# Kernel optimization log

Measured on AMD Instinct MI355X. Metric: run time of the kernel, lower is better.

The kernel has to match this reference:

```python
import jax, jax.numpy as jnp
import numpy as np

PAD = (2, 2)  # from kernel=[1,3,3,1], sampling_factor_padding=2, kernel_size=3


def _make_kernel(k1d):
    k = np.asarray(k1d, dtype=np.float32)
    k2d = k[None, :] * k[:, None]
    return jnp.asarray(k2d / k2d.sum())


def setup_inputs() -> dict:
    key = jax.random.key(0)
    x = jax.random.normal(key, (8, 256, 256, 256), dtype=jnp.float32)
    kernel = _make_kernel([1, 3, 3, 1])  # [4,4] normalized FIR kernel (buffer)
    return {"x": x, "kernel": kernel}


def reference(x, kernel):
    # upfirdn2d with up=1, down=1, pad=(2,2): pad then depthwise TRUE convolution
    # (StyleGAN2 flips the kernel before F.conv2d, i.e. real convolution).
    B, C, H, W = x.shape
    kh, kw = kernel.shape
    w = jnp.flip(kernel, (0, 1)).astype(x.dtype)[None, None]  # [1,1,kh,kw]
    w = jnp.broadcast_to(w, (C, 1, kh, kw))  # depthwise: same kernel per channel
    out = jax.lax.conv_general_dilated(
        x, w,
        window_strides=(1, 1),
        padding=(PAD, PAD),
        dimension_numbers=("NCHW", "OIHW", "NCHW"),
        feature_group_count=C,
    )  # [B, C, H+1, W+1] since H + 4 - 4 + 1 = H + 1
    return out
```

## Files before the change

### kernel.cpp

```cpp
#include <hip/hip_runtime.h>


#define IW 256
#define IH 256
#define OW 257
#define OH 257
#define HSTR 260
#define NSLOT 35

typedef float f4u __attribute__((vector_size(16), aligned(4)));

__device__ __forceinline__ float sbc(float v) {
    return __uint_as_float(__builtin_amdgcn_readfirstlane(__float_as_uint(v)));
}

__global__ __launch_bounds__(512) void blur_fir_kernel(
    const float* __restrict__ x,
    const float* __restrict__ k2d,
    float* __restrict__ out,
    int ntasks, int nstride)
{
    __shared__ float Hs[NSLOT * HSTR];

    const int lane = threadIdx.x & 63;
    const int wv   = threadIdx.x >> 6;

    const float w0 = sbc(k2d[0]);
    const float w1 = sbc(k2d[1]);
    const float w2 = sbc(k2d[2]);
    const float w3 = sbc(k2d[3]);
    const float inv = 1.0f / w0;
    const float v1 = sbc(k2d[4]  * inv);
    const float v2 = sbc(k2d[8]  * inv);
    const float v3 = sbc(k2d[12] * inv);

    const int   c0 = lane << 2;
    const float mL = (lane > 0)  ? 1.0f : 0.0f;
    const float mR = (lane < 63) ? 1.0f : 0.0f;
    const int   lm = (lane > 0)  ? lane - 1 : 0;
    const int   lp = (lane < 63) ? lane + 1 : 63;
    const bool last = (lane == 63);

    for (int t = blockIdx.x; t < ntasks; t += nstride) {
        const int plane = t >> 3;
        const int rg    = t & 7;
        const int a     = rg << 5;
        const float* xp = x + ((size_t)plane << 16);

        __syncthreads();

        #pragma unroll
        for (int j = wv; j < NSLOT; j += 8) {
            const int r = a - 2 + j;
            int rr = min(max(r, 0), IH - 1);
            float4 Bv = *(const float4*)(xp + (rr << 8) + c0);
            float rm = (r >= 0 && r < IH) ? 1.0f : 0.0f;
            float lx = __shfl(Bv.z, lm, 64) * mL;
            float ly = __shfl(Bv.w, lm, 64) * mL;
            float rv = __shfl(Bv.x, lp, 64) * mR;
            float4 h;
            h.x = w0 * Bv.y + w1 * Bv.x + w2 * ly   + w3 * lx;
            h.y = w0 * Bv.z + w1 * Bv.y + w2 * Bv.x + w3 * ly;
            h.z = w0 * Bv.w + w1 * Bv.z + w2 * Bv.y + w3 * Bv.x;
            h.w = w0 * rv   + w1 * Bv.w + w2 * Bv.z + w3 * Bv.y;
            float h4 = (w2 * Bv.w + w3 * Bv.z) * rm;
            h.x *= rm; h.y *= rm; h.z *= rm; h.w *= rm;
            float* hp = Hs + j * HSTR;
            *(float4*)(hp + c0) = h;
            if (last) hp[256] = h4;
        }
        __syncthreads();

        const int j0 = wv << 2;
        const float* hb = Hs + j0 * HSTR + c0;
        float4 h0 = *(const float4*)(hb           );
        float4 h1 = *(const float4*)(hb +     HSTR);
        float4 h2 = *(const float4*)(hb + 2 * HSTR);
        float4 h3 = *(const float4*)(hb + 3 * HSTR);
        float4 h4 = *(const float4*)(hb + 4 * HSTR);
        float4 h5 = *(const float4*)(hb + 5 * HSTR);
        float4 h6 = *(const float4*)(hb + 6 * HSTR);

        auto vcomb = [&](float4 A, float4 B, float4 C, float4 D) -> float4 {
            float4 r;
            r.x = A.x + v1 * B.x + v2 * C.x + v3 * D.x;
            r.y = A.y + v1 * B.y + v2 * C.y + v3 * D.y;
            r.z = A.z + v1 * B.z + v2 * C.z + v3 * D.z;
            r.w = A.w + v1 * B.w + v2 * C.w + v3 * D.w;
            return r;
        };

        float* op = out + (size_t)plane * (OW * OH)
                        + (size_t)(a + (wv << 2)) * OW + c0;
        float4 R0 = vcomb(h3, h2, h1, h0);
        float4 R1 = vcomb(h4, h3, h2, h1);
        float4 R2 = vcomb(h5, h4, h3, h2);
        float4 R3 = vcomb(h6, h5, h4, h3);
        *(f4u*)(op         ) = (f4u){R0.x, R0.y, R0.z, R0.w};
        *(f4u*)(op +     OW) = (f4u){R1.x, R1.y, R1.z, R1.w};
        *(f4u*)(op + 2 * OW) = (f4u){R2.x, R2.y, R2.z, R2.w};
        *(f4u*)(op + 3 * OW) = (f4u){R3.x, R3.y, R3.z, R3.w};
        if (last) {
            const float* sp = Hs + j0 * HSTR + 256;
            float s0 = sp[0],        s1 = sp[HSTR],     s2 = sp[2 * HSTR];
            float s3 = sp[3 * HSTR], s4 = sp[4 * HSTR], s5 = sp[5 * HSTR];
            float s6 = sp[6 * HSTR];
            op[4]          = s3 + v1 * s2 + v2 * s1 + v3 * s0;
            op[OW + 4]     = s4 + v1 * s3 + v2 * s2 + v3 * s1;
            op[2 * OW + 4] = s5 + v1 * s4 + v2 * s3 + v3 * s2;
            op[3 * OW + 4] = s6 + v1 * s5 + v2 * s4 + v3 * s3;
        }

        if (rg == 7 && wv == 7) {
            float4 Hm2 = *(const float4*)(Hs + 32 * HSTR + c0);
            float4 Hm1 = *(const float4*)(Hs + 33 * HSTR + c0);
            float4 R;
            R.x = v2 * Hm1.x + v3 * Hm2.x;
            R.y = v2 * Hm1.y + v3 * Hm2.y;
            R.z = v2 * Hm1.z + v3 * Hm2.z;
            R.w = v2 * Hm1.w + v3 * Hm2.w;
            *(f4u*)(op + 4 * OW) = (f4u){R.x, R.y, R.z, R.w};
            if (last)
                op[4 * OW + 4] = v2 * Hs[33 * HSTR + 256] + v3 * Hs[32 * HSTR + 256];
        }
    }
}

extern "C" void kernel_launch(void* const* d_in, const int* in_sizes, int n_in,
                              void* d_out, int out_size, void* d_ws, size_t ws_size,
                              hipStream_t stream) {
    const float* x   = (const float*)d_in[0];
    const float* k2d = (const float*)d_in[1];
    float* out = (float*)d_out;

    int nplanes = in_sizes[0] >> 16;
    int ntasks  = nplanes * 8;
    int nblocks = 1024;

    blur_fir_kernel<<<nblocks, 512, 0, stream>>>(x, k2d, out, ntasks, nblocks);
}
```

Measured before the change: 210.4 us.

## Prefetch next task's input rows into registers across loop iterations

Software-pipelines the persistent loop. The global loads for the next task are issued right after the shared-memory fill barrier, so they overlap the vertical pass and the output stores of the current task. The horizontal filter is computed in registers before the first barrier. This hides global load latency at the cost of higher register pressure (five float4 prefetch registers plus five horizontal results), which could reduce occupancy at 512 threads.

```diff
diff --git a/kernel.cpp b/kernel.cpp
--- a/kernel.cpp
+++ b/kernel.cpp
@@ -41,35 +41,72 @@
     const int   lp = (lane < 63) ? lane + 1 : 63;
     const bool last = (lane == 63);
 
-    for (int t = blockIdx.x; t < ntasks; t += nstride) {
+    const int  j4ok = (wv + 32 < NSLOT);
+
+    auto issue = [&](int tt, float4& G0, float4& G1, float4& G2,
+                     float4& G3, float4& G4) {
+        const int plane = tt >> 3;
+        const int a     = (tt & 7) << 5;
+        const float* xp = x + ((size_t)plane << 16);
+        auto ld = [&](int j) -> float4 {
+            int r  = a - 2 + j;
+            int rr = min(max(r, 0), IH - 1);
+            return *(const float4*)(xp + (rr << 8) + c0);
+        };
+        G0 = ld(wv);
+        G1 = ld(wv + 8);
+        G2 = ld(wv + 16);
+        G3 = ld(wv + 24);
+        G4 = j4ok ? ld(wv + 32) : G3;
+    };
+
+    int t = blockIdx.x;
+    float4 G0, G1, G2, G3, G4;
+    if (t < ntasks) issue(t, G0, G1, G2, G3, G4);
+
+    for (; t < ntasks; t += nstride) {
         const int plane = t >> 3;
         const int rg    = t & 7;
         const int a     = rg << 5;
-        const float* xp = x + ((size_t)plane << 16);
+
+        float4 Hv[5]; float h4s[5];
+        {
+            auto hc = [&](float4 Bv, int r, float4& h, float& h4) {
+                float rm = (r >= 0 && r < IH) ? 1.0f : 0.0f;
+                float lx = __shfl(Bv.z, lm, 64) * mL;
+                float ly = __shfl(Bv.w, lm, 64) * mL;
+                float rv = __shfl(Bv.x, lp, 64) * mR;
+                h.x = w0 * Bv.y + w1 * Bv.x + w2 * ly   + w3 * lx;
+                h.y = w0 * Bv.z + w1 * Bv.y + w2 * Bv.x + w3 * ly;
+                h.z = w0 * Bv.w + w1 * Bv.z + w2 * Bv.y + w3 * Bv.x;
+                h.w = w0 * rv   + w1 * Bv.w + w2 * Bv.z + w3 * Bv.y;
+                h4  = (w2 * Bv.w + w3 * Bv.z) * rm;
+                h.x *= rm; h.y *= rm; h.z *= rm; h.w *= rm;
+            };
+            hc(G0, a - 2 + wv,      Hv[0], h4s[0]);
+            hc(G1, a - 2 + wv + 8,  Hv[1], h4s[1]);
+            hc(G2, a - 2 + wv + 16, Hv[2], h4s[2]);
+            hc(G3, a - 2 + wv + 24, Hv[3], h4s[3]);
+            hc(G4, a - 2 + wv + 32, Hv[4], h4s[4]);
+        }
 
         __syncthreads();
 
         #pragma unroll
-        for (int j = wv; j < NSLOT; j += 8) {
-            const int r = a - 2 + j;
-            int rr = min(max(r, 0), IH - 1);
-            float4 Bv = *(const float4*)(xp + (rr << 8) + c0);
-            float rm = (r >= 0 && r < IH) ? 1.0f : 0.0f;
-            float lx = __shfl(Bv.z, lm, 64) * mL;
-            float ly = __shfl(Bv.w, lm, 64) * mL;
-            float rv = __shfl(Bv.x, lp, 64) * mR;
-            float4 h;
-            h.x = w0 * Bv.y + w1 * Bv.x + w2 * ly   + w3 * lx;
-            h.y = w0 * Bv.z + w1 * Bv.y + w2 * Bv.x + w3 * ly;
-            h.z = w0 * Bv.w + w1 * Bv.z + w2 * Bv.y + w3 * Bv.x;
-            h.w = w0 * rv   + w1 * Bv.w + w2 * Bv.z + w3 * Bv.y;
-            float h4 = (w2 * Bv.w + w3 * Bv.z) * rm;
-            h.x *= rm; h.y *= rm; h.z *= rm; h.w *= rm;
-            float* hp = Hs + j * HSTR;
-            *(float4*)(hp + c0) = h;
-            if (last) hp[256] = h4;
+        for (int k = 0; k < 5; ++k) {
+            const int j = wv + (k << 3);
+            if (k < 4 || j4ok) {
+                float* hp = Hs + j * HSTR;
+                *(float4*)(hp + c0) = Hv[k];
+                if (last) hp[256] = h4s[k];
+            }
         }
         __syncthreads();
+
+        {
+            int tn = t + nstride;
+            if (tn < ntasks) issue(tn, G0, G1, G2, G3, G4);
+        }
 
         const int j0 = wv << 2;
         const float* hb = Hs + j0 * HSTR + c0;
```

After: 214.9 us. 1.02x slower.

## Stream whole planes per block through a ring buffer of filtered rows

Applied to the files above, without the earlier changes.

Each block now walks an entire plane in eight sequential 32-row chunks instead of taking independent row-group tasks. Horizontally filtered rows live in a 36-slot shared-memory ring, so the three halo rows are reused from the previous chunk rather than reloaded and refiltered. Each chunk's global loads are issued before the barrier, which lets them overlap with other waves still finishing the previous chunk's output. The cost is more modular index arithmetic, uneven per-wave row counts in the first chunk, and fewer independent tasks for the scheduler to spread across the device.

```diff
diff --git a/kernel.cpp b/kernel.cpp
--- a/kernel.cpp
+++ b/kernel.cpp
@@ -6,7 +6,7 @@
 #define OW 257
 #define OH 257
 #define HSTR 260
-#define NSLOT 35
+#define RING 36
 
 typedef float f4u __attribute__((vector_size(16), aligned(4)));
 
@@ -18,9 +18,9 @@
     const float* __restrict__ x,
     const float* __restrict__ k2d,
     float* __restrict__ out,
-    int ntasks, int nstride)
+    int nplanes, int pstride)
 {
-    __shared__ float Hs[NSLOT * HSTR];
+    __shared__ float Hs[RING * HSTR];
 
     const int lane = threadIdx.x & 63;
     const int wv   = threadIdx.x >> 6;
@@ -41,87 +41,113 @@
     const int   lp = (lane < 63) ? lane + 1 : 63;
     const bool last = (lane == 63);
 
-    for (int t = blockIdx.x; t < ntasks; t += nstride) {
-        const int plane = t >> 3;
-        const int rg    = t & 7;
-        const int a     = rg << 5;
-        const float* xp = x + ((size_t)plane << 16);
+    for (int plane = blockIdx.x; plane < nplanes; plane += pstride) {
+        const float* xp   = x   + ((size_t)plane << 16);
+        float*       outp = out + (size_t)plane * (OW * OH);
 
-        __syncthreads();
+        for (int k = 0; k < 8; ++k) {
+            const int a = k << 5;
 
-        #pragma unroll
-        for (int j = wv; j < NSLOT; j += 8) {
-            const int r = a - 2 + j;
-            int rr = min(max(r, 0), IH - 1);
-            float4 Bv = *(const float4*)(xp + (rr << 8) + c0);
-            float rm = (r >= 0 && r < IH) ? 1.0f : 0.0f;
-            float lx = __shfl(Bv.z, lm, 64) * mL;
-            float ly = __shfl(Bv.w, lm, 64) * mL;
-            float rv = __shfl(Bv.x, lp, 64) * mR;
-            float4 h;
-            h.x = w0 * Bv.y + w1 * Bv.x + w2 * ly   + w3 * lx;
-            h.y = w0 * Bv.z + w1 * Bv.y + w2 * Bv.x + w3 * ly;
-            h.z = w0 * Bv.w + w1 * Bv.z + w2 * Bv.y + w3 * Bv.x;
-            h.w = w0 * rv   + w1 * Bv.w + w2 * Bv.z + w3 * Bv.y;
-            float h4 = (w2 * Bv.w + w3 * Bv.z) * rm;
-            h.x *= rm; h.y *= rm; h.z *= rm; h.w *= rm;
-            float* hp = Hs + j * HSTR;
-            *(float4*)(hp + c0) = h;
-            if (last) hp[256] = h4;
-        }
-        __syncthreads();
+            int n0, cnt;
+            if (k == 0) {
+                n0  = (wv < 3) ? (5 * wv - 2) : ((wv << 2) + 1);
+                cnt = (wv < 3) ? 5 : 4;
+            } else {
+                n0  = a + 1 + (wv << 2);
+                cnt = 4;
+            }
 
-        const int j0 = wv << 2;
-        const float* hb = Hs + j0 * HSTR + c0;
-        float4 h0 = *(const float4*)(hb           );
-        float4 h1 = *(const float4*)(hb +     HSTR);
-        float4 h2 = *(const float4*)(hb + 2 * HSTR);
-        float4 h3 = *(const float4*)(hb + 3 * HSTR);
-        float4 h4 = *(const float4*)(hb + 4 * HSTR);
-        float4 h5 = *(const float4*)(hb + 5 * HSTR);
-        float4 h6 = *(const float4*)(hb + 6 * HSTR);
+            float4 Bv[5];
+            #pragma unroll
+            for (int q = 0; q < 5; ++q) {
+                if (q < cnt) {
+                    int r  = n0 + q;
+                    int rr = min(max(r, 0), IH - 1);
+                    Bv[q] = *(const float4*)(xp + (rr << 8) + c0);
+                }
+            }
 
-        auto vcomb = [&](float4 A, float4 B, float4 C, float4 D) -> float4 {
-            float4 r;
-            r.x = A.x + v1 * B.x + v2 * C.x + v3 * D.x;
-            r.y = A.y + v1 * B.y + v2 * C.y + v3 * D.y;
-            r.z = A.z + v1 * B.z + v2 * C.z + v3 * D.z;
-            r.w = A.w + v1 * B.w + v2 * C.w + v3 * D.w;
-            return r;
-        };
+            __syncthreads();
 
-        float* op = out + (size_t)plane * (OW * OH)
-                        + (size_t)(a + (wv << 2)) * OW + c0;
-        float4 R0 = vcomb(h3, h2, h1, h0);
-        float4 R1 = vcomb(h4, h3, h2, h1);
-        float4 R2 = vcomb(h5, h4, h3, h2);
-        float4 R3 = vcomb(h6, h5, h4, h3);
-        *(f4u*)(op         ) = (f4u){R0.x, R0.y, R0.z, R0.w};
-        *(f4u*)(op +     OW) = (f4u){R1.x, R1.y, R1.z, R1.w};
-        *(f4u*)(op + 2 * OW) = (f4u){R2.x, R2.y, R2.z, R2.w};
-        *(f4u*)(op + 3 * OW) = (f4u){R3.x, R3.y, R3.z, R3.w};
-        if (last) {
-            const float* sp = Hs + j0 * HSTR + 256;
-            float s0 = sp[0],        s1 = sp[HSTR],     s2 = sp[2 * HSTR];
-            float s3 = sp[3 * HSTR], s4 = sp[4 * HSTR], s5 = sp[5 * HSTR];
-            float s6 = sp[6 * HSTR];
-            op[4]          = s3 + v1 * s2 + v2 * s1 + v3 * s0;
-            op[OW + 4]     = s4 + v1 * s3 + v2 * s2 + v3 * s1;
-            op[2 * OW + 4] = s5 + v1 * s4 + v2 * s3 + v3 * s2;
-            op[3 * OW + 4] = s6 + v1 * s5 + v2 * s4 + v3 * s3;
-        }
+            const int s0 = (n0 + 2) % RING;
+            #pragma unroll
+            for (int q = 0; q < 5; ++q) {
+                if (q < cnt) {
+                    const int r = n0 + q;
+                    float rm = (r >= 0 && r < IH) ? 1.0f : 0.0f;
+                    float4 B = Bv[q];
+                    float lx = __shfl(B.z, lm, 64) * mL;
+                    float ly = __shfl(B.w, lm, 64) * mL;
+                    float rv = __shfl(B.x, lp, 64) * mR;
+                    float4 h;
+                    h.x = w0 * B.y + w1 * B.x + w2 * ly  + w3 * lx;
+                    h.y = w0 * B.z + w1 * B.y + w2 * B.x + w3 * ly;
+                    h.z = w0 * B.w + w1 * B.z + w2 * B.y + w3 * B.x;
+                    h.w = w0 * rv  + w1 * B.w + w2 * B.z + w3 * B.y;
+                    float h4 = (w2 * B.w + w3 * B.z) * rm;
+                    h.x *= rm; h.y *= rm; h.z *= rm; h.w *= rm;
+                    int sq = s0 + q; if (sq >= RING) sq -= RING;
+                    float* hp = Hs + sq * HSTR;
+                    *(float4*)(hp + c0) = h;
+                    if (last) hp[256] = h4;
+                }
+            }
+            __syncthreads();
 
-        if (rg == 7 && wv == 7) {
-            float4 Hm2 = *(const float4*)(Hs + 32 * HSTR + c0);
-            float4 Hm1 = *(const float4*)(Hs + 33 * HSTR + c0);
-            float4 R;
-            R.x = v2 * Hm1.x + v3 * Hm2.x;
-            R.y = v2 * Hm1.y + v3 * Hm2.y;
-            R.z = v2 * Hm1.z + v3 * Hm2.z;
-            R.w = v2 * Hm1.w + v3 * Hm2.w;
-            *(f4u*)(op + 4 * OW) = (f4u){R.x, R.y, R.z, R.w};
-            if (last)
-                op[4 * OW + 4] = v2 * Hs[33 * HSTR + 256] + v3 * Hs[32 * HSTR + 256];
+            const int t0 = (a + (wv << 2)) % RING;
+            float4 h[7];
+            #pragma unroll
+            for (int q = 0; q < 7; ++q) {
+                int sq = t0 + q; if (sq >= RING) sq -= RING;
+                h[q] = *(const float4*)(Hs + sq * HSTR + c0);
+            }
+
+            auto vcomb = [&](float4 A, float4 B, float4 C, float4 D) -> float4 {
+                float4 r;
+                r.x = A.x + v1 * B.x + v2 * C.x + v3 * D.x;
+                r.y = A.y + v1 * B.y + v2 * C.y + v3 * D.y;
+                r.z = A.z + v1 * B.z + v2 * C.z + v3 * D.z;
+                r.w = A.w + v1 * B.w + v2 * C.w + v3 * D.w;
+                return r;
+            };
+
+            float* op = outp + (size_t)(a + (wv << 2)) * OW + c0;
+            float4 R0 = vcomb(h[3], h[2], h[1], h[0]);
+            float4 R1 = vcomb(h[4], h[3], h[2], h[1]);
+            float4 R2 = vcomb(h[5], h[4], h[3], h[2]);
+            float4 R3 = vcomb(h[6], h[5], h[4], h[3]);
+            *(f4u*)(op         ) = (f4u){R0.x, R0.y, R0.z, R0.w};
+            *(f4u*)(op +     OW) = (f4u){R1.x, R1.y, R1.z, R1.w};
+            *(f4u*)(op + 2 * OW) = (f4u){R2.x, R2.y, R2.z, R2.w};
+            *(f4u*)(op + 3 * OW) = (f4u){R3.x, R3.y, R3.z, R3.w};
+            if (last) {
+                float s[7];
+                #pragma unroll
+                for (int q = 0; q < 7; ++q) {
+                    int sq = t0 + q; if (sq >= RING) sq -= RING;
+                    s[q] = Hs[sq * HSTR + 256];
+                }
+                op[4]          = s[3] + v1 * s[2] + v2 * s[1] + v3 * s[0];
+                op[OW + 4]     = s[4] + v1 * s[3] + v2 * s[2] + v3 * s[1];
+                op[2 * OW + 4] = s[5] + v1 * s[4] + v2 * s[3] + v3 * s[2];
+                op[3 * OW + 4] = s[6] + v1 * s[5] + v2 * s[4] + v3 * s[3];
+            }
+
+            if (k == 7 && wv == 7) {
+                const int sA = 256 % RING;
+                const int sB = 257 % RING;
+                float4 Hm2 = *(const float4*)(Hs + sA * HSTR + c0);
+                float4 Hm1 = *(const float4*)(Hs + sB * HSTR + c0);
+                float4 R;
+                R.x = v2 * Hm1.x + v3 * Hm2.x;
+                R.y = v2 * Hm1.y + v3 * Hm2.y;
+                R.z = v2 * Hm1.z + v3 * Hm2.z;
+                R.w = v2 * Hm1.w + v3 * Hm2.w;
+                float* o2 = outp + (size_t)256 * OW + c0;
+                *(f4u*)o2 = (f4u){R.x, R.y, R.z, R.w};
+                if (last)
+                    o2[4] = v2 * Hs[sB * HSTR + 256] + v3 * Hs[sA * HSTR + 256];
+            }
         }
     }
 }
@@ -134,8 +160,7 @@
     float* out = (float*)d_out;
 
     int nplanes = in_sizes[0] >> 16;
-    int ntasks  = nplanes * 8;
     int nblocks = 1024;
 
-    blur_fir_kernel<<<nblocks, 512, 0, stream>>>(x, k2d, out, ntasks, nblocks);
+    blur_fir_kernel<<<nblocks, 512, 0, stream>>>(x, k2d, out, nplanes, nblocks);
 }
```

Result: no change. 210.9 us (+0.2%).
